# Kernel tuning notes

Hardware: AMD Instinct MI355X
Metric: run time of the kernel (lower is better)

Reference implementation:

```python
import jax, jax.numpy as jnp
import numpy as np

CAPACITY = 1024


def setup_inputs() -> dict:
    T, H, I, E, K = 2048, 1024, 1408, 8, 2
    key = jax.random.key(0)
    k0, k1, k2, k3, k4 = jax.random.split(key, 5)
    hidden_states = jax.random.normal(k0, (T, H), dtype=jnp.float32)
    w1 = jax.random.normal(k1, (E, 2 * I, H), dtype=jnp.float32) * 0.02  # [gate; up]
    w2 = jax.random.normal(k2, (E, H, I), dtype=jnp.float32) * 0.02
    topk_weights = jax.random.uniform(k3, (T, K), dtype=jnp.float32)
    topk_ids = jax.random.randint(k4, (T, K), 0, E, dtype=jnp.int32)
    return {"hidden_states": hidden_states, "w1": w1, "w2": w2,
            "topk_weights": topk_weights, "topk_ids": topk_ids}


def reference(hidden_states, w1, w2, topk_weights, topk_ids):
    # MoE: prepare(dispatch) -> grouped expert GEMM (silu-gated MLP) -> finalize(combine)
    T, H = hidden_states.shape
    E = w1.shape[0]
    I = w2.shape[2]
    K = topk_ids.shape[1]
    C = CAPACITY

    # ---- prepare: dispatch token copies to per-expert buffers ----
    flat_ids = topk_ids.reshape(-1)                       # (T*K,)
    onehot = jax.nn.one_hot(flat_ids, E, dtype=jnp.int32)  # (T*K, E)
    cs = jnp.cumsum(onehot, axis=0)                        # running per-expert counts
    pos = jnp.take_along_axis(cs, flat_ids[:, None], axis=1)[:, 0] - 1  # slot in expert buffer
    keep = pos < C
    pos_c = jnp.where(keep, pos, 0)

    x_flat = jnp.repeat(hidden_states, K, axis=0)          # (T*K, H)
    x_e = jnp.zeros((E, C, H), dtype=hidden_states.dtype)
    x_e = x_e.at[flat_ids, pos_c].add(jnp.where(keep[:, None], x_flat, 0.0))

    # ---- grouped expert GEMM: silu(gate) * up, then down-proj ----
    h = jnp.einsum('ech,eoh->eco', x_e, w1)                # (E, C, 2I)
    gate, up = h[..., :I], h[..., I:]
    act = jax.nn.silu(gate) * up                           # (E, C, I)
    y = jnp.einsum('eci,ehi->ech', act, w2)                # (E, C, H)

    # ---- finalize: gather back, apply router weights, reduce over top-k ----
    y_flat = y[flat_ids, pos_c] * (keep[:, None].astype(y.dtype)) \
             * topk_weights.reshape(-1, 1)                 # (T*K, H)
    out = y_flat.reshape(T, K, H).sum(axis=1)              # (T, H)
    return out.astype(hidden_states.dtype)
```

## Files before the change

kernel.cpp:

```cpp
#include <hip/hip_runtime.h>

#define NE 8
#define CAP 1024
#define HD 1024
#define ID 1408
#define TT 2048

typedef __attribute__((ext_vector_type(8))) short bf16x8;
typedef __attribute__((ext_vector_type(4))) float f32x4;
typedef unsigned short u16;
typedef unsigned int u32;
typedef unsigned long long u64;

__device__ __forceinline__ u16 f2bf(float f) {
  u32 u = __float_as_uint(f);
  u = (u + 0x7fffu + ((u >> 16) & 1u)) >> 16;
  return (u16)u;
}

__device__ __forceinline__ void async_cp16(const void* g, void* l) {
  __builtin_amdgcn_global_load_lds(
      (const __attribute__((address_space(1))) u32*)g,
      (__attribute__((address_space(3))) u32*)l, 16, 0, 0);
}

#define W1_BLKS (2 * ID * NE)
#define W2_BLKS (NE * HD * ID / 4 / 256)
#define X_BLKS (TT * HD / 4 / 256)
__global__ void prep_kernel(const float4* __restrict__ w1, ushort4* __restrict__ bw1,
                            const float4* __restrict__ w2, ushort4* __restrict__ bw2,
                            const float4* __restrict__ x, ushort4* __restrict__ bx,
                            float4* __restrict__ out) {
  int b = blockIdx.x;
  int tid = threadIdx.x;
  if (b < W1_BLKS) {
    int n = b % (2 * ID);
    int e = b / (2 * ID);
    int j = (n < ID) ? n : (n - ID);
    int np = (j >> 4) * 32 + (j & 15) + ((n < ID) ? 0 : 16);
    float4 v = w1[((size_t)e * 2 * ID + n) * (HD / 4) + tid];
    ushort4 o;
    o.x = f2bf(v.x); o.y = f2bf(v.y); o.z = f2bf(v.z); o.w = f2bf(v.w);
    bw1[((size_t)e * 2 * ID + np) * (HD / 4) + tid] = o;
  } else if (b < W1_BLKS + W2_BLKS) {
    size_t i = (size_t)(b - W1_BLKS) * 256 + tid;
    float4 v = w2[i];
    ushort4 o;
    o.x = f2bf(v.x); o.y = f2bf(v.y); o.z = f2bf(v.z); o.w = f2bf(v.w);
    bw2[i] = o;
  } else {
    size_t i = (size_t)(b - W1_BLKS - W2_BLKS) * 256 + tid;
    float4 v = x[i];
    ushort4 o;
    o.x = f2bf(v.x); o.y = f2bf(v.y); o.z = f2bf(v.z); o.w = f2bf(v.w);
    bx[i] = o;
    out[i] = float4{0.f, 0.f, 0.f, 0.f};
  }
}

__global__ void route_kernel(const int* __restrict__ ids, int* __restrict__ rowmap,
                             int* __restrict__ flatpos, int* __restrict__ counts) {
  __shared__ int ids_s[TT * 2];
  __shared__ int sc[256][NE + 1];
  int tid = threadIdx.x;
  for (int i = tid; i < TT * 2; i += 256) ids_s[i] = ids[i];
  __syncthreads();
  int base = tid * 16;
  u64 own64 = 0;
#pragma unroll
  for (int j = 0; j < 16; ++j) own64 += 1ull << (ids_s[base + j] * 8);
  int own[NE];
#pragma unroll
  for (int e = 0; e < NE; ++e) { own[e] = (int)((own64 >> (e * 8)) & 0xff); sc[tid][e] = own[e]; }
  __syncthreads();
  for (int off = 1; off < 256; off <<= 1) {
    int v[NE];
    if (tid >= off) {
#pragma unroll
      for (int e = 0; e < NE; ++e) v[e] = sc[tid - off][e];
    }
    __syncthreads();
    if (tid >= off) {
#pragma unroll
      for (int e = 0; e < NE; ++e) sc[tid][e] += v[e];
    }
    __syncthreads();
  }
  if (tid == 255) {
#pragma unroll
    for (int e = 0; e < NE; ++e) counts[e] = sc[255][e] < CAP ? sc[255][e] : CAP;
  }
  int excl[NE];
#pragma unroll
  for (int e = 0; e < NE; ++e) excl[e] = sc[tid][e] - own[e];
  __syncthreads();
#pragma unroll
  for (int e = 0; e < NE; ++e) sc[tid][e] = excl[e];
#pragma unroll
  for (int j = 0; j < 16; ++j) {
    int f = base + j;
    int e = ids_s[f];
    int p = sc[tid][e]++;
    if (p < CAP) { rowmap[e * CAP + p] = f; flatpos[f] = p; }
    else flatpos[f] = -1;
  }
}

__global__ __launch_bounds__(256) void gemm1_kernel(
    const u16* __restrict__ A, const u16* __restrict__ B, u16* __restrict__ Hb,
    const int* __restrict__ rowmap, const int* __restrict__ counts) {
  int e = blockIdx.x;
  int count = counts[e];
  int m0 = blockIdx.y * 64;
  if (m0 >= count) return;
  int n0 = blockIdx.z * 128;
  int tid = threadIdx.x;
  int lane = tid & 63, wid = tid >> 6;
  int wm = wid >> 1, wn = wid & 1;
  int q = lane >> 4, lm = lane & 15;

  __shared__ __align__(16) char smA[64 * 128];
  __shared__ __align__(16) char smB[128 * 128];

  int rloc = tid >> 3;
  int chs = ((tid & 7) ^ (rloc & 7)) * 8;
  const u16* aP[2];
  const u16* bP[4];
#pragma unroll
  for (int i = 0; i < 2; ++i) {
    int gr = m0 + rloc + 32 * i;
    int f = (gr < count) ? rowmap[e * CAP + gr] : 0;
    aP[i] = A + (size_t)(f >> 1) * HD + chs;
  }
#pragma unroll
  for (int i = 0; i < 4; ++i)
    bP[i] = B + ((size_t)e * 2 * ID + n0 + rloc + 32 * i) * HD + chs;

  f32x4 zero = {0.f, 0.f, 0.f, 0.f};
  f32x4 acc[2][4];
#pragma unroll
  for (int mi = 0; mi < 2; ++mi)
#pragma unroll
    for (int ni = 0; ni < 4; ++ni) acc[mi][ni] = zero;

  for (int kt = 0; kt < HD / 64; ++kt) {
    int ko = kt * 64;
#pragma unroll
    for (int i = 0; i < 2; ++i)
      async_cp16(aP[i] + ko, smA + (i * 256 + tid) * 16);
#pragma unroll
    for (int i = 0; i < 4; ++i)
      async_cp16(bP[i] + ko, smB + (i * 256 + tid) * 16);
    asm volatile("s_waitcnt vmcnt(0)" ::: "memory");
    __syncthreads();
#pragma unroll
    for (int s = 0; s < 2; ++s) {
      bf16x8 af[2], bfr[4];
#pragma unroll
      for (int mi = 0; mi < 2; ++mi) {
        int row = wm * 32 + mi * 16 + lm;
        af[mi] = *(const bf16x8*)(smA + row * 128 + (((s * 4 + q) ^ (lm & 7)) * 16));
      }
#pragma unroll
      for (int ni = 0; ni < 4; ++ni) {
        int row = wn * 64 + ni * 16 + lm;
        bfr[ni] = *(const bf16x8*)(smB + row * 128 + (((s * 4 + q) ^ (lm & 7)) * 16));
      }
#pragma unroll
      for (int mi = 0; mi < 2; ++mi)
#pragma unroll
        for (int ni = 0; ni < 4; ++ni)
          acc[mi][ni] = __builtin_amdgcn_mfma_f32_16x16x32_bf16(af[mi], bfr[ni], acc[mi][ni], 0, 0, 0);
    }
    __syncthreads();
  }

  u16* smOut = (u16*)smB;
#pragma unroll
  for (int mi = 0; mi < 2; ++mi) {
#pragma unroll
    for (int k = 0; k < 2; ++k) {
      int colL = wn * 32 + k * 16 + lm;
#pragma unroll
      for (int r = 0; r < 4; ++r) {
        float g = acc[mi][2 * k][r];
        float u = acc[mi][2 * k + 1][r];
        float a = g / (1.f + __expf(-g)) * u;
        int row = wm * 32 + mi * 16 + q * 4 + r;
        smOut[row * 72 + colL] = f2bf(a);
      }
    }
  }
  __syncthreads();
  {
    int row = tid >> 2, seg = tid & 3;
    const u16* sp = smOut + row * 72 + seg * 16;
    bf16x8 v0 = *(const bf16x8*)sp;
    bf16x8 v1 = *(const bf16x8*)(sp + 8);
    u16* dp = Hb + ((size_t)e * CAP + m0 + row) * ID + (n0 >> 1) + seg * 16;
    *(bf16x8*)dp = v0;
    *(bf16x8*)(dp + 8) = v1;
  }
}

__global__ __launch_bounds__(256) void gemm2_kernel(
    const u16* __restrict__ A, const u16* __restrict__ B, float* __restrict__ out,
    const int* __restrict__ rowmap, const int* __restrict__ counts,
    const float* __restrict__ tw) {
  int e = blockIdx.x;
  int count = counts[e];
  int m0 = blockIdx.y * 64;
  if (m0 >= count) return;
  int n0 = blockIdx.z * 64;
  int tid = threadIdx.x;
  int lane = tid & 63, wid = tid >> 6;
  int wm = wid >> 1, wn = wid & 1;
  int q = lane >> 4, lm = lane & 15;

  __shared__ __align__(16) char smA[64 * 128];
  __shared__ __align__(16) char smB[64 * 128];

  int rloc = tid >> 3;
  int chs = ((tid & 7) ^ (rloc & 7)) * 8;
  const u16* aP[2];
  const u16* bP[2];
#pragma unroll
  for (int i = 0; i < 2; ++i) {
    aP[i] = A + ((size_t)e * CAP + m0 + rloc + 32 * i) * ID + chs;
    bP[i] = B + ((size_t)e * HD + n0 + rloc + 32 * i) * ID + chs;
  }

  f32x4 zero = {0.f, 0.f, 0.f, 0.f};
  f32x4 acc[2][2];
#pragma unroll
  for (int mi = 0; mi < 2; ++mi)
#pragma unroll
    for (int ni = 0; ni < 2; ++ni) acc[mi][ni] = zero;

  for (int kt = 0; kt < ID / 64; ++kt) {
    int ko = kt * 64;
#pragma unroll
    for (int i = 0; i < 2; ++i) {
      async_cp16(aP[i] + ko, smA + (i * 256 + tid) * 16);
      async_cp16(bP[i] + ko, smB + (i * 256 + tid) * 16);
    }
    asm volatile("s_waitcnt vmcnt(0)" ::: "memory");
    __syncthreads();
#pragma unroll
    for (int s = 0; s < 2; ++s) {
      bf16x8 af[2], bfr[2];
#pragma unroll
      for (int mi = 0; mi < 2; ++mi) {
        int row = wm * 32 + mi * 16 + lm;
        af[mi] = *(const bf16x8*)(smA + row * 128 + (((s * 4 + q) ^ (lm & 7)) * 16));
      }
#pragma unroll
      for (int ni = 0; ni < 2; ++ni) {
        int row = wn * 32 + ni * 16 + lm;
        bfr[ni] = *(const bf16x8*)(smB + row * 128 + (((s * 4 + q) ^ (lm & 7)) * 16));
      }
#pragma unroll
      for (int mi = 0; mi < 2; ++mi)
#pragma unroll
        for (int ni = 0; ni < 2; ++ni)
          acc[mi][ni] = __builtin_amdgcn_mfma_f32_16x16x32_bf16(af[mi], bfr[ni], acc[mi][ni], 0, 0, 0);
    }
    __syncthreads();
  }

#pragma unroll
  for (int mi = 0; mi < 2; ++mi) {
#pragma unroll
    for (int r = 0; r < 4; ++r) {
      int grow = m0 + wm * 32 + mi * 16 + q * 4 + r;
      if (grow < count) {
        int f = rowmap[e * CAP + grow];
        float w = tw[f];
        int t = f >> 1;
#pragma unroll
        for (int ni = 0; ni < 2; ++ni) {
          int col = n0 + wn * 32 + ni * 16 + lm;
          atomicAdd(&out[(size_t)t * HD + col], w * acc[mi][ni][r]);
        }
      }
    }
  }
}

extern "C" void kernel_launch(void* const* d_in, const int* in_sizes, int n_in,
                              void* d_out, int out_size, void* d_ws, size_t ws_size,
                              hipStream_t stream) {
  const float* hidden = (const float*)d_in[0];
  const float* w1 = (const float*)d_in[1];
  const float* w2 = (const float*)d_in[2];
  const float* tw = (const float*)d_in[3];
  const int* ids = (const int*)d_in[4];
  float* out = (float*)d_out;

  char* p = (char*)d_ws;
  auto alloc = [&](size_t b) { char* r = p; p += (b + 255) & ~(size_t)255; return r; };
  u16* bw1 = (u16*)alloc((size_t)NE * 2 * ID * HD * 2);
  u16* bw2 = (u16*)alloc((size_t)NE * HD * ID * 2);
  u16* bx = (u16*)alloc((size_t)TT * HD * 2);
  u16* hbuf = (u16*)alloc((size_t)NE * CAP * ID * 2);
  int* rowmap = (int*)alloc((size_t)NE * CAP * 4);
  int* flatpos = (int*)alloc((size_t)TT * 2 * 4);
  int* counts = (int*)alloc((size_t)NE * 4);

  prep_kernel<<<W1_BLKS + W2_BLKS + X_BLKS, 256, 0, stream>>>(
      (const float4*)w1, (ushort4*)bw1, (const float4*)w2, (ushort4*)bw2,
      (const float4*)hidden, (ushort4*)bx, (float4*)out);

  route_kernel<<<1, 256, 0, stream>>>(ids, rowmap, flatpos, counts);

  gemm1_kernel<<<dim3(NE, CAP / 64, 2 * ID / 128), 256, 0, stream>>>(
      bx, bw1, hbuf, rowmap, counts);

  gemm2_kernel<<<dim3(NE, CAP / 64, HD / 64), 256, 0, stream>>>(
      hbuf, bw2, out, rowmap, counts, tw);
}
```

Baseline: 265.9 us.

## Fold routing into prep kernel, widen conversion blocks, enlarge gemm1 M tile

```diff
diff --git a/kernel.cpp b/kernel.cpp
--- a/kernel.cpp
+++ b/kernel.cpp
@@ -18,91 +18,119 @@
   return (u16)u;
 }
 
+__device__ __forceinline__ bf16x8 pack8(float4 a, float4 b) {
+  bf16x8 r;
+  r[0] = (short)f2bf(a.x); r[1] = (short)f2bf(a.y);
+  r[2] = (short)f2bf(a.z); r[3] = (short)f2bf(a.w);
+  r[4] = (short)f2bf(b.x); r[5] = (short)f2bf(b.y);
+  r[6] = (short)f2bf(b.z); r[7] = (short)f2bf(b.w);
+  return r;
+}
+
 __device__ __forceinline__ void async_cp16(const void* g, void* l) {
   __builtin_amdgcn_global_load_lds(
       (const __attribute__((address_space(1))) u32*)g,
       (__attribute__((address_space(3))) u32*)l, 16, 0, 0);
 }
 
-#define W1_BLKS (2 * ID * NE)
-#define W2_BLKS (NE * HD * ID / 4 / 256)
-#define X_BLKS (TT * HD / 4 / 256)
-__global__ void prep_kernel(const float4* __restrict__ w1, ushort4* __restrict__ bw1,
-                            const float4* __restrict__ w2, ushort4* __restrict__ bw2,
-                            const float4* __restrict__ x, ushort4* __restrict__ bx,
-                            float4* __restrict__ out) {
+#define W1B (NE * 2 * ID / 4)
+#define W2B (NE * HD * ID / 4096)
+#define XB (TT * HD / 4096)
+__global__ __launch_bounds__(256) void prep_kernel(
+    const float4* __restrict__ w1, bf16x8* __restrict__ bw1,
+    const float4* __restrict__ w2, bf16x8* __restrict__ bw2,
+    const float4* __restrict__ x, bf16x8* __restrict__ bx,
+    float4* __restrict__ out, const int* __restrict__ ids,
+    int* __restrict__ rowmap, int* __restrict__ counts) {
   int b = blockIdx.x;
   int tid = threadIdx.x;
-  if (b < W1_BLKS) {
-    int n = b % (2 * ID);
-    int e = b / (2 * ID);
+  if (b == 0) {
+    __shared__ unsigned char ids_s[TT * 2];
+    __shared__ int sc[256][NE + 1];
+    for (int i = tid; i < TT * 2; i += 256) ids_s[i] = (unsigned char)ids[i];
+    __syncthreads();
+    int base = tid * 16;
+    u64 own64 = 0;
+#pragma unroll
+    for (int j = 0; j < 16; ++j) own64 += 1ull << (ids_s[base + j] * 8);
+    int own[NE];
+#pragma unroll
+    for (int e = 0; e < NE; ++e) {
+      own[e] = (int)((own64 >> (e * 8)) & 0xff);
+      sc[tid][e] = own[e];
+    }
+    __syncthreads();
+    for (int off = 1; off < 256; off <<= 1) {
+      int v[NE];
+      if (tid >= off) {
+#pragma unroll
+        for (int e = 0; e < NE; ++e) v[e] = sc[tid - off][e];
+      }
+      __syncthreads();
+      if (tid >= off) {
+#pragma unroll
+        for (int e = 0; e < NE; ++e) sc[tid][e] += v[e];
+      }
+      __syncthreads();
+    }
+    if (tid == 255) {
+#pragma unroll
+      for (int e = 0; e < NE; ++e) counts[e] = sc[255][e] < CAP ? sc[255][e] : CAP;
+    }
+    int excl[NE];
+#pragma unroll
+    for (int e = 0; e < NE; ++e) excl[e] = sc[tid][e] - own[e];
+    __syncthreads();
+#pragma unroll
+    for (int e = 0; e < NE; ++e) sc[tid][e] = excl[e];
+#pragma unroll
+    for (int j = 0; j < 16; ++j) {
+      int f = base + j;
+      int e = ids_s[f];
+      int p = sc[tid][e]++;
+      if (p < CAP) rowmap[e * CAP + p] = f;
+    }
+    return;
+  }
+  int bb = b - 1;
+  if (bb < W1B) {
+    int rl = tid >> 6, c = tid & 63;
+    int g = bb * 4 + rl;
+    int e = g / (2 * ID);
+    int n = g - e * (2 * ID);
     int j = (n < ID) ? n : (n - ID);
     int np = (j >> 4) * 32 + (j & 15) + ((n < ID) ? 0 : 16);
-    float4 v = w1[((size_t)e * 2 * ID + n) * (HD / 4) + tid];
-    ushort4 o;
-    o.x = f2bf(v.x); o.y = f2bf(v.y); o.z = f2bf(v.z); o.w = f2bf(v.w);
-    bw1[((size_t)e * 2 * ID + np) * (HD / 4) + tid] = o;
-  } else if (b < W1_BLKS + W2_BLKS) {
-    size_t i = (size_t)(b - W1_BLKS) * 256 + tid;
-    float4 v = w2[i];
-    ushort4 o;
-    o.x = f2bf(v.x); o.y = f2bf(v.y); o.z = f2bf(v.z); o.w = f2bf(v.w);
-    bw2[i] = o;
+    const float4* src = w1 + ((size_t)e * 2 * ID + n) * (HD / 4);
+    bf16x8* dst = bw1 + ((size_t)e * 2 * ID + np) * (HD / 8);
+    float4 v0 = src[c * 2];
+    float4 v1 = src[c * 2 + 1];
+    float4 v2 = src[128 + c * 2];
+    float4 v3 = src[128 + c * 2 + 1];
+    dst[c] = pack8(v0, v1);
+    dst[64 + c] = pack8(v2, v3);
+  } else if (bb < W1B + W2B) {
+    size_t base4 = (size_t)(bb - W1B) * 1024;
+    float4 v0 = w2[base4 + tid * 2];
+    float4 v1 = w2[base4 + tid * 2 + 1];
+    float4 v2 = w2[base4 + 512 + tid * 2];
+    float4 v3 = w2[base4 + 512 + tid * 2 + 1];
+    bf16x8* dst = bw2 + base4 / 2;
+    dst[tid] = pack8(v0, v1);
+    dst[256 + tid] = pack8(v2, v3);
   } else {
-    size_t i = (size_t)(b - W1_BLKS - W2_BLKS) * 256 + tid;
-    float4 v = x[i];
-    ushort4 o;
-    o.x = f2bf(v.x); o.y = f2bf(v.y); o.z = f2bf(v.z); o.w = f2bf(v.w);
-    bx[i] = o;
-    out[i] = float4{0.f, 0.f, 0.f, 0.f};
-  }
-}
-
-__global__ void route_kernel(const int* __restrict__ ids, int* __restrict__ rowmap,
-                             int* __restrict__ flatpos, int* __restrict__ counts) {
-  __shared__ int ids_s[TT * 2];
-  __shared__ int sc[256][NE + 1];
-  int tid = threadIdx.x;
-  for (int i = tid; i < TT * 2; i += 256) ids_s[i] = ids[i];
-  __syncthreads();
-  int base = tid * 16;
-  u64 own64 = 0;
-#pragma unroll
-  for (int j = 0; j < 16; ++j) own64 += 1ull << (ids_s[base + j] * 8);
-  int own[NE];
-#pragma unroll
-  for (int e = 0; e < NE; ++e) { own[e] = (int)((own64 >> (e * 8)) & 0xff); sc[tid][e] = own[e]; }
-  __syncthreads();
-  for (int off = 1; off < 256; off <<= 1) {
-    int v[NE];
-    if (tid >= off) {
-#pragma unroll
-      for (int e = 0; e < NE; ++e) v[e] = sc[tid - off][e];
-    }
-    __syncthreads();
-    if (tid >= off) {
-#pragma unroll
-      for (int e = 0; e < NE; ++e) sc[tid][e] += v[e];
-    }
-    __syncthreads();
-  }
-  if (tid == 255) {
-#pragma unroll
-    for (int e = 0; e < NE; ++e) counts[e] = sc[255][e] < CAP ? sc[255][e] : CAP;
-  }
-  int excl[NE];
-#pragma unroll
-  for (int e = 0; e < NE; ++e) excl[e] = sc[tid][e] - own[e];
-  __syncthreads();
-#pragma unroll
-  for (int e = 0; e < NE; ++e) sc[tid][e] = excl[e];
-#pragma unroll
-  for (int j = 0; j < 16; ++j) {
-    int f = base + j;
-    int e = ids_s[f];
-    int p = sc[tid][e]++;
-    if (p < CAP) { rowmap[e * CAP + p] = f; flatpos[f] = p; }
-    else flatpos[f] = -1;
+    size_t base4 = (size_t)(bb - W1B - W2B) * 1024;
+    float4 v0 = x[base4 + tid * 2];
+    float4 v1 = x[base4 + tid * 2 + 1];
+    float4 v2 = x[base4 + 512 + tid * 2];
+    float4 v3 = x[base4 + 512 + tid * 2 + 1];
+    bf16x8* dst = bx + base4 / 2;
+    dst[tid] = pack8(v0, v1);
+    dst[256 + tid] = pack8(v2, v3);
+    float4 z = {0.f, 0.f, 0.f, 0.f};
+    out[base4 + tid] = z;
+    out[base4 + 256 + tid] = z;
+    out[base4 + 512 + tid] = z;
+    out[base4 + 768 + tid] = z;
   }
 }
 
@@ -111,7 +139,7 @@
     const int* __restrict__ rowmap, const int* __restrict__ counts) {
   int e = blockIdx.x;
   int count = counts[e];
-  int m0 = blockIdx.y * 64;
+  int m0 = blockIdx.y * 128;
   if (m0 >= count) return;
   int n0 = blockIdx.z * 128;
   int tid = threadIdx.x;
@@ -119,34 +147,33 @@
   int wm = wid >> 1, wn = wid & 1;
   int q = lane >> 4, lm = lane & 15;
 
-  __shared__ __align__(16) char smA[64 * 128];
-  __shared__ __align__(16) char smB[128 * 128];
+  __shared__ __align__(16) char sm[32768];
+  char* smA = sm;
+  char* smB = sm + 16384;
 
   int rloc = tid >> 3;
   int chs = ((tid & 7) ^ (rloc & 7)) * 8;
-  const u16* aP[2];
+  const u16* aP[4];
   const u16* bP[4];
 #pragma unroll
-  for (int i = 0; i < 2; ++i) {
+  for (int i = 0; i < 4; ++i) {
     int gr = m0 + rloc + 32 * i;
     int f = (gr < count) ? rowmap[e * CAP + gr] : 0;
     aP[i] = A + (size_t)(f >> 1) * HD + chs;
-  }
-#pragma unroll
-  for (int i = 0; i < 4; ++i)
     bP[i] = B + ((size_t)e * 2 * ID + n0 + rloc + 32 * i) * HD + chs;
+  }
 
   f32x4 zero = {0.f, 0.f, 0.f, 0.f};
-  f32x4 acc[2][4];
-#pragma unroll
-  for (int mi = 0; mi < 2; ++mi)
+  f32x4 acc[4][4];
+#pragma unroll
+  for (int mi = 0; mi < 4; ++mi)
 #pragma unroll
     for (int ni = 0; ni < 4; ++ni) acc[mi][ni] = zero;
 
   for (int kt = 0; kt < HD / 64; ++kt) {
     int ko = kt * 64;
 #pragma unroll
-    for (int i = 0; i < 2; ++i)
+    for (int i = 0; i < 4; ++i)
       async_cp16(aP[i] + ko, smA + (i * 256 + tid) * 16);
 #pragma unroll
     for (int i = 0; i < 4; ++i)
@@ -155,10 +182,10 @@
     __syncthreads();
 #pragma unroll
     for (int s = 0; s < 2; ++s) {
-      bf16x8 af[2], bfr[4];
-#pragma unroll
-      for (int mi = 0; mi < 2; ++mi) {
-        int row = wm * 32 + mi * 16 + lm;
+      bf16x8 af[4], bfr[4];
+#pragma unroll
+      for (int mi = 0; mi < 4; ++mi) {
+        int row = wm * 64 + mi * 16 + lm;
         af[mi] = *(const bf16x8*)(smA + row * 128 + (((s * 4 + q) ^ (lm & 7)) * 16));
       }
 #pragma unroll
@@ -167,7 +194,7 @@
         bfr[ni] = *(const bf16x8*)(smB + row * 128 + (((s * 4 + q) ^ (lm & 7)) * 16));
       }
 #pragma unroll
-      for (int mi = 0; mi < 2; ++mi)
+      for (int mi = 0; mi < 4; ++mi)
 #pragma unroll
         for (int ni = 0; ni < 4; ++ni)
           acc[mi][ni] = __builtin_amdgcn_mfma_f32_16x16x32_bf16(af[mi], bfr[ni], acc[mi][ni], 0, 0, 0);
@@ -175,9 +202,9 @@
     __syncthreads();
   }
 
-  u16* smOut = (u16*)smB;
-#pragma unroll
-  for (int mi = 0; mi < 2; ++mi) {
+  u16* smOut = (u16*)sm;
+#pragma unroll
+  for (int mi = 0; mi < 4; ++mi) {
 #pragma unroll
     for (int k = 0; k < 2; ++k) {
       int colL = wn * 32 + k * 16 + lm;
@@ -186,20 +213,24 @@
         float g = acc[mi][2 * k][r];
         float u = acc[mi][2 * k + 1][r];
         float a = g / (1.f + __expf(-g)) * u;
-        int row = wm * 32 + mi * 16 + q * 4 + r;
+        int row = wm * 64 + mi * 16 + q * 4 + r;
         smOut[row * 72 + colL] = f2bf(a);
       }
     }
   }
   __syncthreads();
   {
-    int row = tid >> 2, seg = tid & 3;
-    const u16* sp = smOut + row * 72 + seg * 16;
+    int row = tid >> 1, seg = tid & 1;
+    const u16* sp = smOut + row * 72 + seg * 32;
     bf16x8 v0 = *(const bf16x8*)sp;
     bf16x8 v1 = *(const bf16x8*)(sp + 8);
-    u16* dp = Hb + ((size_t)e * CAP + m0 + row) * ID + (n0 >> 1) + seg * 16;
+    bf16x8 v2 = *(const bf16x8*)(sp + 16);
+    bf16x8 v3 = *(const bf16x8*)(sp + 24);
+    u16* dp = Hb + ((size_t)e * CAP + m0 + row) * ID + (n0 >> 1) + seg * 32;
     *(bf16x8*)dp = v0;
     *(bf16x8*)(dp + 8) = v1;
+    *(bf16x8*)(dp + 16) = v2;
+    *(bf16x8*)(dp + 24) = v3;
   }
 }
 
@@ -304,16 +335,13 @@
   u16* bx = (u16*)alloc((size_t)TT * HD * 2);
   u16* hbuf = (u16*)alloc((size_t)NE * CAP * ID * 2);
   int* rowmap = (int*)alloc((size_t)NE * CAP * 4);
-  int* flatpos = (int*)alloc((size_t)TT * 2 * 4);
   int* counts = (int*)alloc((size_t)NE * 4);
 
-  prep_kernel<<<W1_BLKS + W2_BLKS + X_BLKS, 256, 0, stream>>>(
-      (const float4*)w1, (ushort4*)bw1, (const float4*)w2, (ushort4*)bw2,
-      (const float4*)hidden, (ushort4*)bx, (float4*)out);
-
-  route_kernel<<<1, 256, 0, stream>>>(ids, rowmap, flatpos, counts);
-
-  gemm1_kernel<<<dim3(NE, CAP / 64, 2 * ID / 128), 256, 0, stream>>>(
+  prep_kernel<<<1 + W1B + W2B + XB, 256, 0, stream>>>(
+      (const float4*)w1, (bf16x8*)bw1, (const float4*)w2, (bf16x8*)bw2,
+      (const float4*)hidden, (bf16x8*)bx, (float4*)out, ids, rowmap, counts);
+
+  gemm1_kernel<<<dim3(NE, CAP / 128, 2 * ID / 128), 256, 0, stream>>>(
       bx, bw1, hbuf, rowmap, counts);
 
   gemm2_kernel<<<dim3(NE, CAP / 64, HD / 64), 256, 0, stream>>>(
```

After: 272.5 us. 2.5% more time.
